# Kernel optimization log

Measured on AMD Instinct MI355X. Metric: run time of the kernel, lower is better.

## Reference

```python
import jax, jax.numpy as jnp
import numpy as np

N_NODES = 50000
N_EDGES = 800000
HIDDEN = 128
HEADS = 8
HEAD_DIM = HIDDEN // HEADS


def setup_inputs() -> dict:
    key = jax.random.key(0)
    ks = jax.random.split(key, 9)
    h = jax.random.normal(ks[0], (N_NODES, HIDDEN), dtype=jnp.float32)
    src = jax.random.randint(ks[1], (N_EDGES,), 0, N_NODES, dtype=jnp.int64)
    dst = jax.random.randint(ks[2], (N_EDGES,), 0, N_NODES, dtype=jnp.int64)
    s = 1.0 / np.sqrt(HIDDEN)
    WQ_w = jax.random.normal(ks[3], (HIDDEN, HIDDEN), dtype=jnp.float32) * s
    WQ_b = jax.random.normal(ks[4], (HIDDEN,), dtype=jnp.float32) * 0.01
    WK_w = jax.random.normal(ks[5], (HIDDEN, HIDDEN), dtype=jnp.float32) * s
    WK_b = jax.random.normal(ks[6], (HIDDEN,), dtype=jnp.float32) * 0.01
    WV_w = jax.random.normal(ks[7], (HIDDEN, HIDDEN), dtype=jnp.float32) * s
    WV_b = jax.random.normal(ks[8], (HIDDEN,), dtype=jnp.float32) * 0.01
    return {"h": h, "src": src, "dst": dst,
            "WQ_w": WQ_w, "WQ_b": WQ_b,
            "WK_w": WK_w, "WK_b": WK_b,
            "WV_w": WV_w, "WV_b": WV_b}


def reference(h, src, dst, WQ_w, WQ_b, WK_w, WK_b, WV_w, WV_b):
    n = h.shape[0]
    scale = jnp.sqrt(jnp.asarray(HEAD_DIM, dtype=h.dtype))
    # QKV projections (torch Linear: x @ W.T + b), reshape to [N, H, D]
    Q = (h @ WQ_w.T + WQ_b).reshape(n, HEADS, HEAD_DIM)
    K = (h @ WK_w.T + WK_b).reshape(n, HEADS, HEAD_DIM)
    V = (h @ WV_w.T + WV_b).reshape(n, HEADS, HEAD_DIM)
    # per-edge scores: (Q[dst] * K[src]).sum(-1) / scale  -> [E, H]
    scores = jnp.einsum("ehd,ehd->eh", Q[dst], K[src]) / scale
    # segment softmax over incoming edges of each dst node
    m = jax.ops.segment_max(scores, dst, num_segments=n)          # [N, H]
    e = jnp.exp(scores - m[dst])                                   # [E, H]
    denom = jax.ops.segment_sum(e, dst, num_segments=n)           # [N, H]
    attn = e / denom[dst]                                          # [E, H]
    # weighted V aggregation: [E,H,1]*[E,H,D] scattered to dst -> [N,H,D]
    out = jax.ops.segment_sum(attn[:, :, None] * V[src], dst, num_segments=n)
    return out  # [N, HEADS, HEAD_DIM]
```

## Files before the change

kernel.cpp:

```cpp
#include <hip/hip_runtime.h>
#include <hip/hip_bf16.h>
#include <cstdint>

#define HID 128
#define NH 8
#define HD 16

typedef __attribute__((ext_vector_type(8))) short bf16x8;
typedef __attribute__((ext_vector_type(4))) float f32x4;

#if __has_builtin(__builtin_amdgcn_exp2f)
#define EXP2(x) __builtin_amdgcn_exp2f(x)
#else
#define EXP2(x) exp2f(x)
#endif

__device__ __forceinline__ short bfr(float x) {
  return (short)__bfloat16_as_ushort(__float2bfloat16(x));
}

__device__ __forceinline__ void up2(uint32_t w, float& lo, float& hi) {
  lo = __uint_as_float(w << 16);
  hi = __uint_as_float(w & 0xffff0000u);
}

__global__ __launch_bounds__(256) void prep_kernel(
    const int* __restrict__ src, const int* __restrict__ dst,
    int* __restrict__ cursors, int* __restrict__ buckets, int E, int C, int FB,
    const float* __restrict__ h,
    const float* __restrict__ W0, const float* __restrict__ b0,
    const float* __restrict__ W1, const float* __restrict__ b1,
    const float* __restrict__ W2, const float* __restrict__ b2,
    ushort* __restrict__ Q, ushort* __restrict__ KV, int n) {
  const int tid = threadIdx.x;

  if (blockIdx.x < (unsigned)FB) {
    int e = blockIdx.x * 256 + tid;
    if (e < E) {
      int d = dst[e];
      int pos = atomicAdd(&cursors[d], 1);
      if (pos < C) buckets[(size_t)d * C + pos] = src[e];
    }
    return;
  }

  __shared__ short As[16 * 64 * 8];
  const int m0 = (blockIdx.x - FB) * 64;

  {
    const int row = tid >> 2, q = tid & 3;
    const int gm = m0 + row;
    const bool ok = gm < n;
    const float4* hp = (const float4*)(h + (size_t)gm * HID + q * 32);
#pragma unroll
    for (int j2 = 0; j2 < 4; ++j2) {
      float4 a = ok ? hp[2 * j2] : make_float4(0.f, 0.f, 0.f, 0.f);
      float4 b = ok ? hp[2 * j2 + 1] : make_float4(0.f, 0.f, 0.f, 0.f);
      bf16x8 c;
      c[0] = bfr(a.x); c[1] = bfr(a.y); c[2] = bfr(a.z); c[3] = bfr(a.w);
      c[4] = bfr(b.x); c[5] = bfr(b.y); c[6] = bfr(b.z); c[7] = bfr(b.w);
      int ch = q * 4 + j2;
      *(bf16x8*)&As[(ch * 64 + row) * 8] = c;
    }
  }
  __syncthreads();

  const int lane = tid & 63;
  const int w = tid >> 6;
  const int r16 = lane & 15;
  const int kg = lane >> 4;

  const float* Wms[3] = {W0, W1, W2};
  const float* bms[3] = {b0, b1, b2};

#pragma unroll
  for (int mat = 0; mat < 3; ++mat) {
    const float* Wm = Wms[mat];
    f32x4 acc[2][4] = {};
#pragma unroll
    for (int ks = 0; ks < 4; ++ks) {
      bf16x8 wfrag[2];
#pragma unroll
      for (int ct = 0; ct < 2; ++ct) {
        const int gr = w * 32 + ct * 16 + r16;
        const float* wrow = Wm + (size_t)gr * HID + ks * 32 + kg * 8;
        float4 wa = *(const float4*)wrow;
        float4 wb = *(const float4*)(wrow + 4);
        bf16x8 wf;
        wf[0] = bfr(wa.x); wf[1] = bfr(wa.y); wf[2] = bfr(wa.z); wf[3] = bfr(wa.w);
        wf[4] = bfr(wb.x); wf[5] = bfr(wb.y); wf[6] = bfr(wb.z); wf[7] = bfr(wb.w);
        wfrag[ct] = wf;
      }
#pragma unroll
      for (int rt = 0; rt < 4; ++rt) {
        bf16x8 hfrag = *(const bf16x8*)&As[((ks * 4 + kg) * 64 + rt * 16 + r16) * 8];
#pragma unroll
        for (int ct = 0; ct < 2; ++ct)
          acc[ct][rt] = __builtin_amdgcn_mfma_f32_16x16x32_bf16(wfrag[ct], hfrag, acc[ct][rt], 0, 0, 0);
      }
    }
    const float* bm = bms[mat];
    ushort* base = (mat == 0) ? Q : (mat == 1) ? KV : (KV + HID);
    const int rs = (mat == 0) ? HID : 2 * HID;
#pragma unroll
    for (int ct = 0; ct < 2; ++ct) {
      const int col0 = w * 32 + ct * 16 + kg * 4;
      const float4 bias = *(const float4*)(bm + col0);
#pragma unroll
      for (int rt = 0; rt < 4; ++rt) {
        int gm = m0 + rt * 16 + r16;
        if (gm < n) {
          float c0 = acc[ct][rt][0] + bias.x;
          float c1 = acc[ct][rt][1] + bias.y;
          float c2 = acc[ct][rt][2] + bias.z;
          float c3 = acc[ct][rt][3] + bias.w;
          uint2 u;
          u.x = (uint32_t)__bfloat16_as_ushort(__float2bfloat16(c0)) |
                ((uint32_t)__bfloat16_as_ushort(__float2bfloat16(c1)) << 16);
          u.y = (uint32_t)__bfloat16_as_ushort(__float2bfloat16(c2)) |
                ((uint32_t)__bfloat16_as_ushort(__float2bfloat16(c3)) << 16);
          *(uint2*)(base + (size_t)gm * rs + col0) = u;
        }
      }
    }
  }
}

__global__ __launch_bounds__(256) void agg_kernel(
    const char* __restrict__ Qb, const char* __restrict__ KVb,
    const int* __restrict__ cursors, const int* __restrict__ buckets, int C,
    float* __restrict__ out, int n) {
  const int tid = threadIdx.x;
  const int lane = tid & 63;
  const int node = blockIdx.x * 4 + (tid >> 6);
  if (node >= n) return;

  const int q = lane >> 4;
  const int sub = lane & 15;
  const int so = sub << 4;

  const float S = 0.25f * 1.44269504f;
  uint4 qw = *(const uint4*)(Qb + (((size_t)node) << 8) + so);
  float qf0, qf1, qf2, qf3, qf4, qf5, qf6, qf7;
  up2(qw.x, qf0, qf1); up2(qw.y, qf2, qf3);
  up2(qw.z, qf4, qf5); up2(qw.w, qf6, qf7);
  qf0 *= S; qf1 *= S; qf2 *= S; qf3 *= S;
  qf4 *= S; qf5 *= S; qf6 *= S; qf7 *= S;

  const int deg = min(cursors[node], C);
  const int* bk = buckets + (size_t)node * C;
  int2 myidx = *(const int2*)(bk + ((sub & 7) << 3) + (q << 1));

  float m_r = -1e30f, sum_r = 0.f;
  float a0 = 0.f, a1 = 0.f, a2 = 0.f, a3 = 0.f;
  float a4 = 0.f, a5 = 0.f, a6 = 0.f, a7 = 0.f;

  const int nit = (deg + 7) >> 3;
  for (int it = 0; it < nit; ++it) {
    const int srcl = (lane & 48) | it;
    const int i0 = __shfl(myidx.x, srcl);
    const int i1 = __shfl(myidx.y, srcl);
    const int e0 = it * 8 + 2 * q, e1 = e0 + 1;
    const uint32_t s0 = min((uint32_t)i0, (uint32_t)(n - 1));
    const uint32_t s1 = min((uint32_t)i1, (uint32_t)(n - 1));
    const size_t rb0 = ((size_t)s0) << 9;
    const size_t rb1 = ((size_t)s1) << 9;
    const uint4 k0 = *(const uint4*)(KVb + rb0 + so);
    const uint4 k1 = *(const uint4*)(KVb + rb1 + so);
    const uint4 v0w = *(const uint4*)(KVb + rb0 + 256 + so);
    const uint4 v1w = *(const uint4*)(KVb + rb1 + 256 + so);

    float x0, x1;
    up2(k0.x, x0, x1); float p0 = qf0 * x0 + qf1 * x1;
    up2(k0.y, x0, x1); p0 += qf2 * x0 + qf3 * x1;
    up2(k0.z, x0, x1); p0 += qf4 * x0 + qf5 * x1;
    up2(k0.w, x0, x1); p0 += qf6 * x0 + qf7 * x1;
    up2(k1.x, x0, x1); float p1 = qf0 * x0 + qf1 * x1;
    up2(k1.y, x0, x1); p1 += qf2 * x0 + qf3 * x1;
    up2(k1.z, x0, x1); p1 += qf4 * x0 + qf5 * x1;
    up2(k1.w, x0, x1); p1 += qf6 * x0 + qf7 * x1;
    p0 += __shfl_xor(p0, 1);
    p1 += __shfl_xor(p1, 1);
    p0 = (e0 < deg) ? p0 : -INFINITY;
    p1 = (e1 < deg) ? p1 : -INFINITY;

    const float mn = fmaxf(m_r, fmaxf(p0, p1));
    const float scale = EXP2(m_r - mn);
    const float w0 = EXP2(p0 - mn);
    const float w1 = EXP2(p1 - mn);
    m_r = mn;
    sum_r = sum_r * scale + w0 + w1;
    float y0, y1, z0, z1;
    up2(v0w.x, y0, y1); up2(v1w.x, z0, z1);
    a0 = a0 * scale + w0 * y0 + w1 * z0; a1 = a1 * scale + w0 * y1 + w1 * z1;
    up2(v0w.y, y0, y1); up2(v1w.y, z0, z1);
    a2 = a2 * scale + w0 * y0 + w1 * z0; a3 = a3 * scale + w0 * y1 + w1 * z1;
    up2(v0w.z, y0, y1); up2(v1w.z, z0, z1);
    a4 = a4 * scale + w0 * y0 + w1 * z0; a5 = a5 * scale + w0 * y1 + w1 * z1;
    up2(v0w.w, y0, y1); up2(v1w.w, z0, z1);
    a6 = a6 * scale + w0 * y0 + w1 * z0; a7 = a7 * scale + w0 * y1 + w1 * z1;
  }

  float mo = fmaxf(m_r, __shfl_xor(m_r, 16));
  mo = fmaxf(mo, __shfl_xor(mo, 32));
  const float sc = EXP2(m_r - mo);
  float s_all = sum_r * sc;
  s_all += __shfl_xor(s_all, 16);
  s_all += __shfl_xor(s_all, 32);
  a0 *= sc; a1 *= sc; a2 *= sc; a3 *= sc;
  a4 *= sc; a5 *= sc; a6 *= sc; a7 *= sc;
  a0 += __shfl_xor(a0, 16); a1 += __shfl_xor(a1, 16);
  a2 += __shfl_xor(a2, 16); a3 += __shfl_xor(a3, 16);
  a4 += __shfl_xor(a4, 16); a5 += __shfl_xor(a5, 16);
  a6 += __shfl_xor(a6, 16); a7 += __shfl_xor(a7, 16);
  a0 += __shfl_xor(a0, 32); a1 += __shfl_xor(a1, 32);
  a2 += __shfl_xor(a2, 32); a3 += __shfl_xor(a3, 32);
  a4 += __shfl_xor(a4, 32); a5 += __shfl_xor(a5, 32);
  a6 += __shfl_xor(a6, 32); a7 += __shfl_xor(a7, 32);

  if (q == 0) {
    const float inv = (s_all > 0.f) ? 1.f / s_all : 0.f;
    float* orow = out + (((size_t)node) << 7) + (sub << 3);
    *(float4*)orow = make_float4(a0 * inv, a1 * inv, a2 * inv, a3 * inv);
    *(float4*)(orow + 4) = make_float4(a4 * inv, a5 * inv, a6 * inv, a7 * inv);
  }
}


extern "C" void kernel_launch(void* const* d_in, const int* in_sizes, int n_in,
                              void* d_out, int out_size, void* d_ws, size_t ws_size,
                              hipStream_t stream) {
  const float* h  = (const float*)d_in[0];
  const int* src  = (const int*)d_in[1];
  const int* dst  = (const int*)d_in[2];
  const float* WQ = (const float*)d_in[3];
  const float* bQ = (const float*)d_in[4];
  const float* WK = (const float*)d_in[5];
  const float* bK = (const float*)d_in[6];
  const float* WV = (const float*)d_in[7];
  const float* bV = (const float*)d_in[8];
  float* out = (float*)d_out;

  const int n = in_sizes[0] / HID;
  const int E = in_sizes[1];
  const int FB = (E + 255) / 256;
  const int QB = (n + 63) / 64;

  ushort* Q  = (ushort*)d_ws;
  ushort* KV = Q + (size_t)n * HID;
  int* cursors = (int*)(KV + (size_t)n * 2 * HID);
  int* buckets = cursors + n;

  const size_t fixed = (size_t)n * (HID + 2 * HID) * 2 + (size_t)n * 4;
  int C = 64;
  if (fixed + ((size_t)n * 64 + 64) * 4 > ws_size) C = 48;
  if (fixed + ((size_t)n * 48 + 64) * 4 > ws_size) C = 40;

  hipMemsetAsync(cursors, 0, (size_t)n * sizeof(int), stream);
  prep_kernel<<<FB + QB, 256, 0, stream>>>(src, dst, cursors, buckets, E, C, FB,
                                           h, WQ, bQ, WK, bK, WV, bV, Q, KV, n);
  agg_kernel<<<(n + 3) / 4, 256, 0, stream>>>((const char*)Q, (const char*)KV,
                                              cursors, buckets, C, out, n);
}
```

Measured before the change: 169.8 us.

## Interleave bucket and projection blocks; process four edges per lane in aggregation

The prep kernel now interleaves blocks in groups of four, three doing the edge-bucketing scatter and one doing the QKV projection tile, so both kinds of work run concurrently instead of all bucketing blocks launching first. The aggregation kernel now handles 16 edges per iteration (4 per lane quarter) instead of 8. Each lane issues four K/V gathers per iteration, which raises memory-level parallelism and halves the number of online-softmax rescales. The cost is higher register pressure from holding eight uint4 loads, which may reduce occupancy, and more wasted work on the padded tail for low-degree nodes.

```diff
diff --git a/kernel.cpp b/kernel.cpp
--- a/kernel.cpp
+++ b/kernel.cpp
@@ -24,28 +24,44 @@
   hi = __uint_as_float(w & 0xffff0000u);
 }
 
+__device__ __forceinline__ float dotq(const uint4 k, const float* qf) {
+  float x0, x1, p;
+  up2(k.x, x0, x1); p  = qf[0] * x0 + qf[1] * x1;
+  up2(k.y, x0, x1); p += qf[2] * x0 + qf[3] * x1;
+  up2(k.z, x0, x1); p += qf[4] * x0 + qf[5] * x1;
+  up2(k.w, x0, x1); p += qf[6] * x0 + qf[7] * x1;
+  return p;
+}
+
 __global__ __launch_bounds__(256) void prep_kernel(
     const int* __restrict__ src, const int* __restrict__ dst,
-    int* __restrict__ cursors, int* __restrict__ buckets, int E, int C, int FB,
+    int* __restrict__ cursors, int* __restrict__ buckets, int E, int C,
+    int FB, int QB,
     const float* __restrict__ h,
     const float* __restrict__ W0, const float* __restrict__ b0,
     const float* __restrict__ W1, const float* __restrict__ b1,
     const float* __restrict__ W2, const float* __restrict__ b2,
     ushort* __restrict__ Q, ushort* __restrict__ KV, int n) {
+  __shared__ short As[16 * 64 * 8];
   const int tid = threadIdx.x;
-
-  if (blockIdx.x < (unsigned)FB) {
-    int e = blockIdx.x * 256 + tid;
-    if (e < E) {
-      int d = dst[e];
-      int pos = atomicAdd(&cursors[d], 1);
-      if (pos < C) buckets[(size_t)d * C + pos] = src[e];
+  const int g = blockIdx.x >> 2;
+  const int r = blockIdx.x & 3;
+
+  if (r != 3) {
+    const int fb = g * 3 + r;
+    if (fb < FB) {
+      const int e = fb * 256 + tid;
+      if (e < E) {
+        int d = dst[e];
+        int pos = atomicAdd(&cursors[d], 1);
+        if (pos < C) buckets[(size_t)d * C + pos] = src[e];
+      }
     }
     return;
   }
 
-  __shared__ short As[16 * 64 * 8];
-  const int m0 = (blockIdx.x - FB) * 64;
+  if (g >= QB) return;
+  const int m0 = g * 64;
 
   {
     const int row = tid >> 2, q = tid & 3;
@@ -141,64 +157,60 @@
 
   const float S = 0.25f * 1.44269504f;
   uint4 qw = *(const uint4*)(Qb + (((size_t)node) << 8) + so);
-  float qf0, qf1, qf2, qf3, qf4, qf5, qf6, qf7;
-  up2(qw.x, qf0, qf1); up2(qw.y, qf2, qf3);
-  up2(qw.z, qf4, qf5); up2(qw.w, qf6, qf7);
-  qf0 *= S; qf1 *= S; qf2 *= S; qf3 *= S;
-  qf4 *= S; qf5 *= S; qf6 *= S; qf7 *= S;
+  float qf[8];
+  up2(qw.x, qf[0], qf[1]); up2(qw.y, qf[2], qf[3]);
+  up2(qw.z, qf[4], qf[5]); up2(qw.w, qf[6], qf[7]);
+#pragma unroll
+  for (int i = 0; i < 8; ++i) qf[i] *= S;
 
   const int deg = min(cursors[node], C);
   const int* bk = buckets + (size_t)node * C;
-  int2 myidx = *(const int2*)(bk + ((sub & 7) << 3) + (q << 1));
+  int4 myidx = *(const int4*)(bk + (sub << 2));
 
   float m_r = -1e30f, sum_r = 0.f;
-  float a0 = 0.f, a1 = 0.f, a2 = 0.f, a3 = 0.f;
-  float a4 = 0.f, a5 = 0.f, a6 = 0.f, a7 = 0.f;
-
-  const int nit = (deg + 7) >> 3;
+  float a[8] = {};
+
+  const int nit = (deg + 15) >> 4;
   for (int it = 0; it < nit; ++it) {
-    const int srcl = (lane & 48) | it;
-    const int i0 = __shfl(myidx.x, srcl);
-    const int i1 = __shfl(myidx.y, srcl);
-    const int e0 = it * 8 + 2 * q, e1 = e0 + 1;
-    const uint32_t s0 = min((uint32_t)i0, (uint32_t)(n - 1));
-    const uint32_t s1 = min((uint32_t)i1, (uint32_t)(n - 1));
-    const size_t rb0 = ((size_t)s0) << 9;
-    const size_t rb1 = ((size_t)s1) << 9;
-    const uint4 k0 = *(const uint4*)(KVb + rb0 + so);
-    const uint4 k1 = *(const uint4*)(KVb + rb1 + so);
-    const uint4 v0w = *(const uint4*)(KVb + rb0 + 256 + so);
-    const uint4 v1w = *(const uint4*)(KVb + rb1 + 256 + so);
-
-    float x0, x1;
-    up2(k0.x, x0, x1); float p0 = qf0 * x0 + qf1 * x1;
-    up2(k0.y, x0, x1); p0 += qf2 * x0 + qf3 * x1;
-    up2(k0.z, x0, x1); p0 += qf4 * x0 + qf5 * x1;
-    up2(k0.w, x0, x1); p0 += qf6 * x0 + qf7 * x1;
-    up2(k1.x, x0, x1); float p1 = qf0 * x0 + qf1 * x1;
-    up2(k1.y, x0, x1); p1 += qf2 * x0 + qf3 * x1;
-    up2(k1.z, x0, x1); p1 += qf4 * x0 + qf5 * x1;
-    up2(k1.w, x0, x1); p1 += qf6 * x0 + qf7 * x1;
-    p0 += __shfl_xor(p0, 1);
-    p1 += __shfl_xor(p1, 1);
-    p0 = (e0 < deg) ? p0 : -INFINITY;
-    p1 = (e1 < deg) ? p1 : -INFINITY;
-
-    const float mn = fmaxf(m_r, fmaxf(p0, p1));
+    const int srcl = (lane & 48) | (it * 4 + q);
+    int idx[4];
+    idx[0] = __shfl(myidx.x, srcl);
+    idx[1] = __shfl(myidx.y, srcl);
+    idx[2] = __shfl(myidx.z, srcl);
+    idx[3] = __shfl(myidx.w, srcl);
+    const int eb = it * 16 + 4 * q;
+    uint4 kw[4], vw[4];
+#pragma unroll
+    for (int j = 0; j < 4; ++j) {
+      const uint32_t s = min((uint32_t)idx[j], (uint32_t)(n - 1));
+      const size_t rb = ((size_t)s) << 9;
+      kw[j] = *(const uint4*)(KVb + rb + so);
+      vw[j] = *(const uint4*)(KVb + rb + 256 + so);
+    }
+    float p[4];
+#pragma unroll
+    for (int j = 0; j < 4; ++j) {
+      float t = dotq(kw[j], qf);
+      t += __shfl_xor(t, 1);
+      p[j] = (eb + j < deg) ? t : -INFINITY;
+    }
+    const float mn = fmaxf(fmaxf(fmaxf(p[0], p[1]), fmaxf(p[2], p[3])), m_r);
     const float scale = EXP2(m_r - mn);
-    const float w0 = EXP2(p0 - mn);
-    const float w1 = EXP2(p1 - mn);
+    float wv[4];
+#pragma unroll
+    for (int j = 0; j < 4; ++j) wv[j] = EXP2(p[j] - mn);
     m_r = mn;
-    sum_r = sum_r * scale + w0 + w1;
-    float y0, y1, z0, z1;
-    up2(v0w.x, y0, y1); up2(v1w.x, z0, z1);
-    a0 = a0 * scale + w0 * y0 + w1 * z0; a1 = a1 * scale + w0 * y1 + w1 * z1;
-    up2(v0w.y, y0, y1); up2(v1w.y, z0, z1);
-    a2 = a2 * scale + w0 * y0 + w1 * z0; a3 = a3 * scale + w0 * y1 + w1 * z1;
-    up2(v0w.z, y0, y1); up2(v1w.z, z0, z1);
-    a4 = a4 * scale + w0 * y0 + w1 * z0; a5 = a5 * scale + w0 * y1 + w1 * z1;
-    up2(v0w.w, y0, y1); up2(v1w.w, z0, z1);
-    a6 = a6 * scale + w0 * y0 + w1 * z0; a7 = a7 * scale + w0 * y1 + w1 * z1;
+    sum_r = sum_r * scale + (wv[0] + wv[1]) + (wv[2] + wv[3]);
+#pragma unroll
+    for (int i = 0; i < 8; ++i) a[i] *= scale;
+#pragma unroll
+    for (int j = 0; j < 4; ++j) {
+      float lo, hi;
+      up2(vw[j].x, lo, hi); a[0] += wv[j] * lo; a[1] += wv[j] * hi;
+      up2(vw[j].y, lo, hi); a[2] += wv[j] * lo; a[3] += wv[j] * hi;
+      up2(vw[j].z, lo, hi); a[4] += wv[j] * lo; a[5] += wv[j] * hi;
+      up2(vw[j].w, lo, hi); a[6] += wv[j] * lo; a[7] += wv[j] * hi;
+    }
   }
 
   float mo = fmaxf(m_r, __shfl_xor(m_r, 16));
@@ -207,22 +219,18 @@
   float s_all = sum_r * sc;
   s_all += __shfl_xor(s_all, 16);
   s_all += __shfl_xor(s_all, 32);
-  a0 *= sc; a1 *= sc; a2 *= sc; a3 *= sc;
-  a4 *= sc; a5 *= sc; a6 *= sc; a7 *= sc;
-  a0 += __shfl_xor(a0, 16); a1 += __shfl_xor(a1, 16);
-  a2 += __shfl_xor(a2, 16); a3 += __shfl_xor(a3, 16);
-  a4 += __shfl_xor(a4, 16); a5 += __shfl_xor(a5, 16);
-  a6 += __shfl_xor(a6, 16); a7 += __shfl_xor(a7, 16);
-  a0 += __shfl_xor(a0, 32); a1 += __shfl_xor(a1, 32);
-  a2 += __shfl_xor(a2, 32); a3 += __shfl_xor(a3, 32);
-  a4 += __shfl_xor(a4, 32); a5 += __shfl_xor(a5, 32);
-  a6 += __shfl_xor(a6, 32); a7 += __shfl_xor(a7, 32);
+#pragma unroll
+  for (int i = 0; i < 8; ++i) {
+    a[i] *= sc;
+    a[i] += __shfl_xor(a[i], 16);
+    a[i] += __shfl_xor(a[i], 32);
+  }
 
   if (q == 0) {
     const float inv = (s_all > 0.f) ? 1.f / s_all : 0.f;
     float* orow = out + (((size_t)node) << 7) + (sub << 3);
-    *(float4*)orow = make_float4(a0 * inv, a1 * inv, a2 * inv, a3 * inv);
-    *(float4*)(orow + 4) = make_float4(a4 * inv, a5 * inv, a6 * inv, a7 * inv);
+    *(float4*)orow = make_float4(a[0] * inv, a[1] * inv, a[2] * inv, a[3] * inv);
+    *(float4*)(orow + 4) = make_float4(a[4] * inv, a[5] * inv, a[6] * inv, a[7] * inv);
   }
 }
 
@@ -243,21 +251,22 @@
 
   const int n = in_sizes[0] / HID;
   const int E = in_sizes[1];
-  const int FB = (E + 255) / 256;
-  const int QB = (n + 63) / 64;
 
   ushort* Q  = (ushort*)d_ws;
   ushort* KV = Q + (size_t)n * HID;
   int* cursors = (int*)(KV + (size_t)n * 2 * HID);
   int* buckets = cursors + n;
 
-  const size_t fixed = (size_t)n * (HID + 2 * HID) * 2 + (size_t)n * 4;
+  const size_t fixed = (size_t)n * 384 * 2 + (size_t)n * 4;
   int C = 64;
   if (fixed + ((size_t)n * 64 + 64) * 4 > ws_size) C = 48;
   if (fixed + ((size_t)n * 48 + 64) * 4 > ws_size) C = 40;
 
+  const int FB = (E + 255) / 256;
+  const int QB = (n + 63) / 64;
+  const int GRP = max((FB + 2) / 3, QB);
   hipMemsetAsync(cursors, 0, (size_t)n * sizeof(int), stream);
-  prep_kernel<<<FB + QB, 256, 0, stream>>>(src, dst, cursors, buckets, E, C, FB,
+  prep_kernel<<<GRP * 4, 256, 0, stream>>>(src, dst, cursors, buckets, E, C, FB, QB,
                                            h, WQ, bQ, WK, bK, WV, bV, Q, KV, n);
   agg_kernel<<<(n + 3) / 4, 256, 0, stream>>>((const char*)Q, (const char*)KV,
                                               cursors, buckets, C, out, n);
```

New measurement: 195.1 us. 14.9% more time.
